# Performance work log

Measured on AMD Instinct MI355X. Metric: run time of the kernel, lower is better.

Reference implementation:

```python
import jax, jax.numpy as jnp
import numpy as np

NUM_EMBEDDINGS = 512
EMBEDDING_DIM = 64
COMMITMENT_COST = 0.25


def setup_inputs() -> dict:
    key = jax.random.key(0)
    k_in, k_cb = jax.random.split(key)
    inputs = jax.random.normal(k_in, (32, EMBEDDING_DIM, 64, 64), dtype=jnp.float32)
    # nn.Embedding weight initialized uniform(-1/K, 1/K)
    codebook = jax.random.uniform(
        k_cb, (NUM_EMBEDDINGS, EMBEDDING_DIM), dtype=jnp.float32,
        minval=-1.0 / NUM_EMBEDDINGS, maxval=1.0 / NUM_EMBEDDINGS)
    return {"inputs": inputs, "codebook": codebook}


def reference(inputs, codebook):
    N, D, H, W = inputs.shape
    # [N, H, W, D] -> [N*H*W, D]
    flat = jnp.transpose(inputs, (0, 2, 3, 1)).reshape(-1, D)
    # Squared euclidean distances (argmin identical to cdist's euclidean argmin)
    d2 = (jnp.sum(flat * flat, axis=1, keepdims=True)
          - 2.0 * flat @ codebook.T
          + jnp.sum(codebook * codebook, axis=1))  # [N*H*W, K]
    encoding_index = jnp.argmin(d2, axis=1)  # [N*H*W]
    quantized = codebook[encoding_index]      # gather [N*H*W, D]
    quantized = quantized.reshape(N, H, W, D).transpose(0, 3, 1, 2)  # [N, D, H, W]
    e_latent_loss = jnp.mean((jax.lax.stop_gradient(quantized) - inputs) ** 2)
    q_latent_loss = jnp.mean((quantized - jax.lax.stop_gradient(inputs)) ** 2)
    c_loss = q_latent_loss + COMMITMENT_COST * e_latent_loss
    # straight-through estimator
    quantized_st = inputs + jax.lax.stop_gradient(quantized - inputs)
    return (c_loss, quantized_st)
```

## Files before the change

### kernel.cpp

```cpp
#include <hip/hip_runtime.h>

#define DIM 64
#define HW 4096
#define NELEM 8388608.0f
#define NBLK 1024

typedef __attribute__((ext_vector_type(8))) short short8;
typedef __attribute__((ext_vector_type(4))) float f32x4;
typedef __attribute__((ext_vector_type(2))) float f32x2;

__device__ __forceinline__ unsigned short f2bf(float f) {
  unsigned int u = __builtin_bit_cast(unsigned int, f);
  u += 0x7fffu + ((u >> 16) & 1u);
  return (unsigned short)(u >> 16);
}

__device__ __forceinline__ float wave_sum(float v) {
  #pragma unroll
  for (int off = 32; off >= 1; off >>= 1) v += __shfl_xor(v, off);
  return v;
}


__global__ void vq_prep(const float* __restrict__ CB,
                        unsigned short* __restrict__ aFg,
                        float* __restrict__ cn) {
  const int t = threadIdx.x;
  const int s = blockIdx.x * 512 + t;
  const int chunk = s >> 7, ks = (s >> 6) & 1, ls = s & 63;
  const int code = chunk * 16 + (ls & 15);
  const int d0 = ks * 32 + (ls >> 4) * 8;
  const float* cp = CB + code * DIM + d0;
  float4 u0 = *(const float4*)cp;
  float4 u1 = *(const float4*)(cp + 4);
  short8 p;
  p[0]=(short)f2bf(-2.f*u0.x); p[1]=(short)f2bf(-2.f*u0.y);
  p[2]=(short)f2bf(-2.f*u0.z); p[3]=(short)f2bf(-2.f*u0.w);
  p[4]=(short)f2bf(-2.f*u1.x); p[5]=(short)f2bf(-2.f*u1.y);
  p[6]=(short)f2bf(-2.f*u1.z); p[7]=(short)f2bf(-2.f*u1.w);
  *(short8*)&aFg[s * 8] = p;
  if (blockIdx.x == 0) {
    const float* c2 = CB + t * DIM;
    float sn = 0.f;
    #pragma unroll
    for (int i = 0; i < 16; ++i) {
      float4 u = *(const float4*)(c2 + i * 4);
      sn += u.x*u.x + u.y*u.y + u.z*u.z + u.w*u.w;
    }
    cn[t] = sn;
  }
}

__global__ __launch_bounds__(256, 4)
void vq_main(const float* __restrict__ X, const float* __restrict__ CB,
             const unsigned short* __restrict__ aFg,
             const float* __restrict__ cng,
             float* __restrict__ out,
             float* __restrict__ pA, float* __restrict__ pB) {
  __shared__ __align__(16) unsigned short XF[16 * 64 * 8];
  __shared__ float mW[4][128];
  __shared__ float red[8];

  const int t   = threadIdx.x;
  const int bid = blockIdx.x;
  const int L   = ((bid & 7) << 7) | (bid >> 3);
  const int n   = L >> 5;
  const int hw0 = (L & 31) << 7;
  const int wv  = t >> 6, lane = t & 63;
  const int g   = lane >> 4, lcol = lane & 15;

  const float* Xg = X + n * (DIM * HW) + hw0;

  const int db8 = t >> 5;
  const int cp  = t & 31;
  const int kss = db8 >> 2, gs = db8 & 3;
  f32x2 v[2][8];
  #pragma unroll
  for (int h = 0; h < 2; ++h)
    #pragma unroll
    for (int j = 0; j < 8; ++j)
      v[h][j] = __builtin_nontemporal_load(
          (const f32x2*)(Xg + (db8 * 8 + j) * HW + h * 64 + cp * 2));
  float sx2 = 0.f;
  #pragma unroll
  for (int h = 0; h < 2; ++h)
    #pragma unroll
    for (int j = 0; j < 8; ++j)
      sx2 += v[h][j].x * v[h][j].x + v[h][j].y * v[h][j].y;
  #pragma unroll
  for (int h = 0; h < 2; ++h) {
    #pragma unroll
    for (int ci = 0; ci < 2; ++ci) {
      const int cl   = cp * 2 + ci;
      const int cb   = h * 4 + (cl >> 4);
      const int slot = (cb * 2 + kss) * 64 + gs * 16 + (cl & 15);
      const int swz  = slot ^ ((slot >> 3) & 7);
      short8 w;
      #pragma unroll
      for (int j = 0; j < 8; ++j)
        w[j] = (short)f2bf(ci ? v[h][j].y : v[h][j].x);
      *(short8*)&XF[swz * 8] = w;
    }
  }
  __syncthreads();

  const int swzl = lane ^ ((lane >> 3) & 7);
  short8 bfrag[2][4][2];
  #pragma unroll
  for (int h = 0; h < 2; ++h)
    #pragma unroll
    for (int cb2 = 0; cb2 < 4; ++cb2)
      #pragma unroll
      for (int ks = 0; ks < 2; ++ks)
        bfrag[h][cb2][ks] =
            *(const short8*)&XF[(((h * 4 + cb2) * 2 + ks) * 64 + swzl) * 8];

  float m1[8];
  #pragma unroll
  for (int cb = 0; cb < 8; ++cb) m1[cb] = 3.0e38f;

  const int chunk0 = wv * 8;
  #pragma unroll 2
  for (int i = 0; i < 8; ++i) {
    const int chunk = chunk0 + i;
    const short8 a0 = *(const short8*)&aFg[((chunk*2 + 0) * 64 + lane) * 8];
    const short8 a1 = *(const short8*)&aFg[((chunk*2 + 1) * 64 + lane) * 8];
    const int codebase = chunk * 16 + g * 4;
    const f32x4 cn = *(const f32x4*)&cng[codebase];
    #pragma unroll
    for (int h = 0; h < 2; ++h) {
      #pragma unroll
      for (int cb2 = 0; cb2 < 4; ++cb2) {
        f32x4 acc = cn;
        acc = __builtin_amdgcn_mfma_f32_16x16x32_bf16(a0, bfrag[h][cb2][0], acc, 0, 0, 0);
        acc = __builtin_amdgcn_mfma_f32_16x16x32_bf16(a1, bfrag[h][cb2][1], acc, 0, 0, 0);
        #pragma unroll
        for (int r = 0; r < 4; ++r) {
          unsigned int vb = __builtin_bit_cast(unsigned int, acc[r]);
          vb = (vb & 0xFFFFFE00u) | ((unsigned)(codebase + r) & 0x1FFu);
          m1[h * 4 + cb2] = fminf(m1[h * 4 + cb2], __builtin_bit_cast(float, vb));
        }
      }
    }
  }

  #pragma unroll
  for (int cb = 0; cb < 8; ++cb) {
    m1[cb] = fminf(m1[cb], __shfl_xor(m1[cb], 16));
    m1[cb] = fminf(m1[cb], __shfl_xor(m1[cb], 32));
    if (g == 0) mW[wv][cb * 16 + lcol] = m1[cb];
  }
  __syncthreads();

  float msum = 0.f;
  #pragma unroll
  for (int h = 0; h < 2; ++h) {
    const int c = h * 64 + lane;
    const float p = fminf(fminf(mW[0][c], mW[1][c]),
                          fminf(mW[2][c], mW[3][c]));
    const unsigned int b = __builtin_bit_cast(unsigned int, p);
    const int k = (int)(b & 511u);
    msum += __builtin_bit_cast(float, b & 0xFFFFFE00u);

    const float* cq = CB + k * DIM + wv * 16;
    float* op = out + 1 + n * (DIM * HW) + hw0 + c;
    #pragma unroll
    for (int i = 0; i < 4; ++i) {
      float4 u = *(const float4*)(cq + i * 4);
      __builtin_nontemporal_store(u.x, &op[(wv*16 + i*4 + 0) * HW]);
      __builtin_nontemporal_store(u.y, &op[(wv*16 + i*4 + 1) * HW]);
      __builtin_nontemporal_store(u.z, &op[(wv*16 + i*4 + 2) * HW]);
      __builtin_nontemporal_store(u.w, &op[(wv*16 + i*4 + 3) * HW]);
    }
  }

  float w1 = wave_sum(sx2);
  if (lane == 0) red[wv] = w1;
  if (wv == 0) {
    float w2 = wave_sum(msum);
    if (lane == 0) red[4] = w2;
  }
  __syncthreads();
  if (t == 0) {
    pA[bid] = red[0] + red[1] + red[2] + red[3];
    pB[bid] = red[4];
  }
}

__global__ void vq_fin(const float* __restrict__ pA,
                       const float* __restrict__ pB,
                       float* __restrict__ out) {
  const int t = threadIdx.x;
  f32x2 a = *(const f32x2*)&pA[t * 2];
  f32x2 c = *(const f32x2*)&pB[t * 2];
  float v = a.x + a.y + c.x + c.y;
  v = wave_sum(v);
  __shared__ float r[8];
  if ((t & 63) == 0) r[t >> 6] = v;
  __syncthreads();
  if (t == 0) {
    float s = 0.f;
    #pragma unroll
    for (int i = 0; i < 8; ++i) s += r[i];
    out[0] = 1.25f * s * (1.0f / NELEM);
  }
}

extern "C" void kernel_launch(void* const* d_in, const int* in_sizes, int n_in,
                              void* d_out, int out_size, void* d_ws, size_t ws_size,
                              hipStream_t stream) {
  const float* X  = (const float*)d_in[0];
  const float* CB = (const float*)d_in[1];
  float* out = (float*)d_out;
  char* ws = (char*)d_ws;
  unsigned short* aFg = (unsigned short*)ws;
  float* cn = (float*)(ws + 65536);
  float* pA = (float*)(ws + 67584);
  float* pB = (float*)(ws + 75776);
  (void)in_sizes; (void)n_in; (void)out_size; (void)ws_size;

  vq_prep<<<8, 512, 0, stream>>>(CB, aFg, cn);
  vq_main<<<NBLK, 256, 0, stream>>>(X, CB, aFg, cn, out, pA, pB);
  vq_fin<<<1, 512, 0, stream>>>(pA, pB, out);
}
```

Baseline: 34.25 us.

## Fuse codebook prep into main kernel, keep A fragments and norms in registers

Removes the separate vq_prep launch. Each block now loads its wave's codebook slice from global memory, converts it to bf16 MFMA A-fragments, and computes code norms with a shuffle reduction, all kept in registers. The loop is reordered so the h loop is outermost, which halves the live B fragments, and launch bounds drop to 3 blocks per SM to fit the extra registers. This saves one kernel launch and the workspace round trip, but every block redoes the codebook conversion and occupancy is lower.

```diff
diff --git a/kernel.cpp b/kernel.cpp
--- a/kernel.cpp
+++ b/kernel.cpp
@@ -22,39 +22,8 @@
 }
 
 
-__global__ void vq_prep(const float* __restrict__ CB,
-                        unsigned short* __restrict__ aFg,
-                        float* __restrict__ cn) {
-  const int t = threadIdx.x;
-  const int s = blockIdx.x * 512 + t;
-  const int chunk = s >> 7, ks = (s >> 6) & 1, ls = s & 63;
-  const int code = chunk * 16 + (ls & 15);
-  const int d0 = ks * 32 + (ls >> 4) * 8;
-  const float* cp = CB + code * DIM + d0;
-  float4 u0 = *(const float4*)cp;
-  float4 u1 = *(const float4*)(cp + 4);
-  short8 p;
-  p[0]=(short)f2bf(-2.f*u0.x); p[1]=(short)f2bf(-2.f*u0.y);
-  p[2]=(short)f2bf(-2.f*u0.z); p[3]=(short)f2bf(-2.f*u0.w);
-  p[4]=(short)f2bf(-2.f*u1.x); p[5]=(short)f2bf(-2.f*u1.y);
-  p[6]=(short)f2bf(-2.f*u1.z); p[7]=(short)f2bf(-2.f*u1.w);
-  *(short8*)&aFg[s * 8] = p;
-  if (blockIdx.x == 0) {
-    const float* c2 = CB + t * DIM;
-    float sn = 0.f;
-    #pragma unroll
-    for (int i = 0; i < 16; ++i) {
-      float4 u = *(const float4*)(c2 + i * 4);
-      sn += u.x*u.x + u.y*u.y + u.z*u.z + u.w*u.w;
-    }
-    cn[t] = sn;
-  }
-}
-
-__global__ __launch_bounds__(256, 4)
+__global__ __launch_bounds__(256, 3)
 void vq_main(const float* __restrict__ X, const float* __restrict__ CB,
-             const unsigned short* __restrict__ aFg,
-             const float* __restrict__ cng,
              float* __restrict__ out,
              float* __restrict__ pA, float* __restrict__ pB) {
   __shared__ __align__(16) unsigned short XF[16 * 64 * 8];
@@ -81,6 +50,32 @@
     for (int j = 0; j < 8; ++j)
       v[h][j] = __builtin_nontemporal_load(
           (const f32x2*)(Xg + (db8 * 8 + j) * HW + h * 64 + cp * 2));
+
+  short8 areg[8][2];
+  float cnv[8];
+  #pragma unroll
+  for (int i = 0; i < 8; ++i) {
+    const int code = (wv * 8 + i) * 16 + lcol;
+    float pc = 0.f;
+    #pragma unroll
+    for (int ks = 0; ks < 2; ++ks) {
+      const float* cpp = CB + code * DIM + ks * 32 + g * 8;
+      float4 u0 = *(const float4*)cpp;
+      float4 u1 = *(const float4*)(cpp + 4);
+      pc += u0.x*u0.x + u0.y*u0.y + u0.z*u0.z + u0.w*u0.w
+          + u1.x*u1.x + u1.y*u1.y + u1.z*u1.z + u1.w*u1.w;
+      short8 p;
+      p[0]=(short)f2bf(-2.f*u0.x); p[1]=(short)f2bf(-2.f*u0.y);
+      p[2]=(short)f2bf(-2.f*u0.z); p[3]=(short)f2bf(-2.f*u0.w);
+      p[4]=(short)f2bf(-2.f*u1.x); p[5]=(short)f2bf(-2.f*u1.y);
+      p[6]=(short)f2bf(-2.f*u1.z); p[7]=(short)f2bf(-2.f*u1.w);
+      areg[i][ks] = p;
+    }
+    pc += __shfl_xor(pc, 16);
+    pc += __shfl_xor(pc, 32);
+    cnv[i] = pc;
+  }
+
   float sx2 = 0.f;
   #pragma unroll
   for (int h = 0; h < 2; ++h)
@@ -104,36 +99,34 @@
   }
   __syncthreads();
 
+  float m1[8];
+  #pragma unroll
+  for (int cb = 0; cb < 8; ++cb) m1[cb] = 3.0e38f;
+
   const int swzl = lane ^ ((lane >> 3) & 7);
-  short8 bfrag[2][4][2];
-  #pragma unroll
-  for (int h = 0; h < 2; ++h)
+  #pragma unroll
+  for (int h = 0; h < 2; ++h) {
+    short8 bfrag[4][2];
     #pragma unroll
     for (int cb2 = 0; cb2 < 4; ++cb2)
       #pragma unroll
       for (int ks = 0; ks < 2; ++ks)
-        bfrag[h][cb2][ks] =
+        bfrag[cb2][ks] =
             *(const short8*)&XF[(((h * 4 + cb2) * 2 + ks) * 64 + swzl) * 8];
 
-  float m1[8];
-  #pragma unroll
-  for (int cb = 0; cb < 8; ++cb) m1[cb] = 3.0e38f;
-
-  const int chunk0 = wv * 8;
-  #pragma unroll 2
-  for (int i = 0; i < 8; ++i) {
-    const int chunk = chunk0 + i;
-    const short8 a0 = *(const short8*)&aFg[((chunk*2 + 0) * 64 + lane) * 8];
-    const short8 a1 = *(const short8*)&aFg[((chunk*2 + 1) * 64 + lane) * 8];
-    const int codebase = chunk * 16 + g * 4;
-    const f32x4 cn = *(const f32x4*)&cng[codebase];
-    #pragma unroll
-    for (int h = 0; h < 2; ++h) {
+    #pragma unroll
+    for (int i = 0; i < 8; ++i) {
+      const int codebase = (wv * 8 + i) * 16 + g * 4;
+      f32x4 cn;
+      cn[0] = __shfl(cnv[i], g * 4 + 0, 16);
+      cn[1] = __shfl(cnv[i], g * 4 + 1, 16);
+      cn[2] = __shfl(cnv[i], g * 4 + 2, 16);
+      cn[3] = __shfl(cnv[i], g * 4 + 3, 16);
       #pragma unroll
       for (int cb2 = 0; cb2 < 4; ++cb2) {
         f32x4 acc = cn;
-        acc = __builtin_amdgcn_mfma_f32_16x16x32_bf16(a0, bfrag[h][cb2][0], acc, 0, 0, 0);
-        acc = __builtin_amdgcn_mfma_f32_16x16x32_bf16(a1, bfrag[h][cb2][1], acc, 0, 0, 0);
+        acc = __builtin_amdgcn_mfma_f32_16x16x32_bf16(areg[i][0], bfrag[cb2][0], acc, 0, 0, 0);
+        acc = __builtin_amdgcn_mfma_f32_16x16x32_bf16(areg[i][1], bfrag[cb2][1], acc, 0, 0, 0);
         #pragma unroll
         for (int r = 0; r < 4; ++r) {
           unsigned int vb = __builtin_bit_cast(unsigned int, acc[r]);
@@ -213,13 +206,10 @@
   const float* CB = (const float*)d_in[1];
   float* out = (float*)d_out;
   char* ws = (char*)d_ws;
-  unsigned short* aFg = (unsigned short*)ws;
-  float* cn = (float*)(ws + 65536);
-  float* pA = (float*)(ws + 67584);
-  float* pB = (float*)(ws + 75776);
+  float* pA = (float*)ws;
+  float* pB = (float*)(ws + 4096);
   (void)in_sizes; (void)n_in; (void)out_size; (void)ws_size;
 
-  vq_prep<<<8, 512, 0, stream>>>(CB, aFg, cn);
-  vq_main<<<NBLK, 256, 0, stream>>>(X, CB, aFg, cn, out, pA, pB);
+  vq_main<<<NBLK, 256, 0, stream>>>(X, CB, out, pA, pB);
   vq_fin<<<1, 512, 0, stream>>>(pA, pB, out);
 }
```

Result: slower. 103.1 us (+200.9%).

## Enlarge per-block tile to 512 pixels with 8 waves splitting codebook

Applied to the files above, without the earlier changes.

Each block now handles 512 spatial positions with 512 threads instead of 128 positions with 256 threads, so only 256 blocks run. Each of the 8 waves owns 64 codes and keeps its A fragments and code norms in registers while it loops over 8 column groups. The aim is to reuse the codebook fragments across more pixels and cut how often aFg is refetched per block. Fewer blocks on a 256-CU part gives about one block per CU, which risks poorer latency hiding and higher LDS use per block.

```diff
diff --git a/kernel.cpp b/kernel.cpp
--- a/kernel.cpp
+++ b/kernel.cpp
@@ -3,7 +3,7 @@
 #define DIM 64
 #define HW 4096
 #define NELEM 8388608.0f
-#define NBLK 1024
+#define NBLK 256
 
 typedef __attribute__((ext_vector_type(8))) short short8;
 typedef __attribute__((ext_vector_type(4))) float f32x4;
@@ -51,126 +51,133 @@
   }
 }
 
-__global__ __launch_bounds__(256, 4)
+__global__ __launch_bounds__(512, 2)
 void vq_main(const float* __restrict__ X, const float* __restrict__ CB,
              const unsigned short* __restrict__ aFg,
              const float* __restrict__ cng,
              float* __restrict__ out,
              float* __restrict__ pA, float* __restrict__ pB) {
-  __shared__ __align__(16) unsigned short XF[16 * 64 * 8];
-  __shared__ float mW[4][128];
-  __shared__ float red[8];
+  __shared__ __align__(16) unsigned short XF[64 * 64 * 8];
+  __shared__ float mW[8][512];
+  __shared__ float red[16];
 
   const int t   = threadIdx.x;
   const int bid = blockIdx.x;
-  const int L   = ((bid & 7) << 7) | (bid >> 3);
-  const int n   = L >> 5;
-  const int hw0 = (L & 31) << 7;
+  const int L   = ((bid & 7) << 5) | (bid >> 3);
+  const int n   = L >> 3;
+  const int hw0 = (L & 7) << 9;
   const int wv  = t >> 6, lane = t & 63;
   const int g   = lane >> 4, lcol = lane & 15;
+  const int db8 = t >> 6;
+  const int cs  = lane;
+  const int kss = db8 >> 2, gs = db8 & 3;
 
   const float* Xg = X + n * (DIM * HW) + hw0;
 
-  const int db8 = t >> 5;
-  const int cp  = t & 31;
-  const int kss = db8 >> 2, gs = db8 & 3;
-  f32x2 v[2][8];
-  #pragma unroll
-  for (int h = 0; h < 2; ++h)
-    #pragma unroll
-    for (int j = 0; j < 8; ++j)
-      v[h][j] = __builtin_nontemporal_load(
-          (const f32x2*)(Xg + (db8 * 8 + j) * HW + h * 64 + cp * 2));
+  f32x2 v[8][4];
+  #pragma unroll
+  for (int j = 0; j < 8; ++j)
+    #pragma unroll
+    for (int q = 0; q < 4; ++q)
+      v[j][q] = __builtin_nontemporal_load(
+          (const f32x2*)(Xg + (db8 * 8 + j) * HW + q * 128 + cs * 2));
   float sx2 = 0.f;
   #pragma unroll
-  for (int h = 0; h < 2; ++h)
-    #pragma unroll
-    for (int j = 0; j < 8; ++j)
-      sx2 += v[h][j].x * v[h][j].x + v[h][j].y * v[h][j].y;
-  #pragma unroll
-  for (int h = 0; h < 2; ++h) {
+  for (int j = 0; j < 8; ++j)
+    #pragma unroll
+    for (int q = 0; q < 4; ++q)
+      sx2 += v[j][q].x * v[j][q].x + v[j][q].y * v[j][q].y;
+  #pragma unroll
+  for (int q = 0; q < 4; ++q) {
     #pragma unroll
     for (int ci = 0; ci < 2; ++ci) {
-      const int cl   = cp * 2 + ci;
-      const int cb   = h * 4 + (cl >> 4);
-      const int slot = (cb * 2 + kss) * 64 + gs * 16 + (cl & 15);
+      const int c    = q * 128 + cs * 2 + ci;
+      const int cb   = c >> 4;
+      const int slot = (cb * 2 + kss) * 64 + gs * 16 + (c & 15);
       const int swz  = slot ^ ((slot >> 3) & 7);
       short8 w;
       #pragma unroll
       for (int j = 0; j < 8; ++j)
-        w[j] = (short)f2bf(ci ? v[h][j].y : v[h][j].x);
+        w[j] = (short)f2bf(ci ? v[j][q].y : v[j][q].x);
       *(short8*)&XF[swz * 8] = w;
     }
   }
   __syncthreads();
 
   const int swzl = lane ^ ((lane >> 3) & 7);
-  short8 bfrag[2][4][2];
-  #pragma unroll
-  for (int h = 0; h < 2; ++h)
+  f32x4 cnq[4];
+  #pragma unroll
+  for (int i = 0; i < 4; ++i)
+    cnq[i] = *(const f32x4*)&cng[(wv * 4 + i) * 16 + g * 4];
+
+  #pragma unroll 1
+  for (int cg = 0; cg < 8; ++cg) {
+    short8 bfrag[4][2];
     #pragma unroll
     for (int cb2 = 0; cb2 < 4; ++cb2)
       #pragma unroll
       for (int ks = 0; ks < 2; ++ks)
-        bfrag[h][cb2][ks] =
-            *(const short8*)&XF[(((h * 4 + cb2) * 2 + ks) * 64 + swzl) * 8];
-
-  float m1[8];
-  #pragma unroll
-  for (int cb = 0; cb < 8; ++cb) m1[cb] = 3.0e38f;
-
-  const int chunk0 = wv * 8;
-  #pragma unroll 2
-  for (int i = 0; i < 8; ++i) {
-    const int chunk = chunk0 + i;
-    const short8 a0 = *(const short8*)&aFg[((chunk*2 + 0) * 64 + lane) * 8];
-    const short8 a1 = *(const short8*)&aFg[((chunk*2 + 1) * 64 + lane) * 8];
-    const int codebase = chunk * 16 + g * 4;
-    const f32x4 cn = *(const f32x4*)&cng[codebase];
-    #pragma unroll
-    for (int h = 0; h < 2; ++h) {
+        bfrag[cb2][ks] =
+            *(const short8*)&XF[(((cg * 4 + cb2) * 2 + ks) * 64 + swzl) * 8];
+
+    float m1[4];
+    #pragma unroll
+    for (int cb2 = 0; cb2 < 4; ++cb2) m1[cb2] = 3.0e38f;
+
+    #pragma unroll
+    for (int i = 0; i < 4; ++i) {
+      const int chunk = wv * 4 + i;
+      const short8 a0 = *(const short8*)&aFg[((chunk*2 + 0) * 64 + lane) * 8];
+      const short8 a1 = *(const short8*)&aFg[((chunk*2 + 1) * 64 + lane) * 8];
+      const int codebase = chunk * 16 + g * 4;
       #pragma unroll
       for (int cb2 = 0; cb2 < 4; ++cb2) {
-        f32x4 acc = cn;
-        acc = __builtin_amdgcn_mfma_f32_16x16x32_bf16(a0, bfrag[h][cb2][0], acc, 0, 0, 0);
-        acc = __builtin_amdgcn_mfma_f32_16x16x32_bf16(a1, bfrag[h][cb2][1], acc, 0, 0, 0);
+        f32x4 acc = cnq[i];
+        acc = __builtin_amdgcn_mfma_f32_16x16x32_bf16(a0, bfrag[cb2][0], acc, 0, 0, 0);
+        acc = __builtin_amdgcn_mfma_f32_16x16x32_bf16(a1, bfrag[cb2][1], acc, 0, 0, 0);
         #pragma unroll
         for (int r = 0; r < 4; ++r) {
           unsigned int vb = __builtin_bit_cast(unsigned int, acc[r]);
           vb = (vb & 0xFFFFFE00u) | ((unsigned)(codebase + r) & 0x1FFu);
-          m1[h * 4 + cb2] = fminf(m1[h * 4 + cb2], __builtin_bit_cast(float, vb));
+          m1[cb2] = fminf(m1[cb2], __builtin_bit_cast(float, vb));
         }
       }
     }
-  }
-
-  #pragma unroll
-  for (int cb = 0; cb < 8; ++cb) {
-    m1[cb] = fminf(m1[cb], __shfl_xor(m1[cb], 16));
-    m1[cb] = fminf(m1[cb], __shfl_xor(m1[cb], 32));
-    if (g == 0) mW[wv][cb * 16 + lcol] = m1[cb];
+    #pragma unroll
+    for (int cb2 = 0; cb2 < 4; ++cb2) {
+      m1[cb2] = fminf(m1[cb2], __shfl_xor(m1[cb2], 16));
+      m1[cb2] = fminf(m1[cb2], __shfl_xor(m1[cb2], 32));
+      if (g == 0) mW[wv][cg * 64 + cb2 * 16 + lcol] = m1[cb2];
+    }
   }
   __syncthreads();
 
   float msum = 0.f;
-  #pragma unroll
-  for (int h = 0; h < 2; ++h) {
-    const int c = h * 64 + lane;
-    const float p = fminf(fminf(mW[0][c], mW[1][c]),
-                          fminf(mW[2][c], mW[3][c]));
+  const float* cqp[8];
+  #pragma unroll
+  for (int hh = 0; hh < 8; ++hh) {
+    const int c = hh * 64 + lane;
+    float p = fminf(fminf(mW[0][c], mW[1][c]), fminf(mW[2][c], mW[3][c]));
+    p = fminf(p, fminf(fminf(mW[4][c], mW[5][c]), fminf(mW[6][c], mW[7][c])));
     const unsigned int b = __builtin_bit_cast(unsigned int, p);
     const int k = (int)(b & 511u);
     msum += __builtin_bit_cast(float, b & 0xFFFFFE00u);
-
-    const float* cq = CB + k * DIM + wv * 16;
-    float* op = out + 1 + n * (DIM * HW) + hw0 + c;
-    #pragma unroll
-    for (int i = 0; i < 4; ++i) {
-      float4 u = *(const float4*)(cq + i * 4);
-      __builtin_nontemporal_store(u.x, &op[(wv*16 + i*4 + 0) * HW]);
-      __builtin_nontemporal_store(u.y, &op[(wv*16 + i*4 + 1) * HW]);
-      __builtin_nontemporal_store(u.z, &op[(wv*16 + i*4 + 2) * HW]);
-      __builtin_nontemporal_store(u.w, &op[(wv*16 + i*4 + 3) * HW]);
+    cqp[hh] = CB + k * DIM + wv * 8;
+  }
+
+  float* opb = out + 1 + n * (DIM * HW) + hw0 + lane;
+  #pragma unroll
+  for (int i = 0; i < 2; ++i) {
+    f32x4 U[8];
+    #pragma unroll
+    for (int hh = 0; hh < 8; ++hh)
+      U[hh] = *(const f32x4*)(cqp[hh] + i * 4);
+    #pragma unroll
+    for (int rr = 0; rr < 4; ++rr) {
+      float* op = opb + (wv * 8 + i * 4 + rr) * HW;
+      #pragma unroll
+      for (int hh = 0; hh < 8; ++hh)
+        __builtin_nontemporal_store(U[hh][rr], &op[hh * 64]);
     }
   }
 
@@ -178,12 +185,15 @@
   if (lane == 0) red[wv] = w1;
   if (wv == 0) {
     float w2 = wave_sum(msum);
-    if (lane == 0) red[4] = w2;
+    if (lane == 0) red[8] = w2;
   }
   __syncthreads();
   if (t == 0) {
-    pA[bid] = red[0] + red[1] + red[2] + red[3];
-    pB[bid] = red[4];
+    float s = 0.f;
+    #pragma unroll
+    for (int i = 0; i < 8; ++i) s += red[i];
+    pA[bid] = s;
+    pB[bid] = red[8];
   }
 }
 
@@ -191,19 +201,13 @@
                        const float* __restrict__ pB,
                        float* __restrict__ out) {
   const int t = threadIdx.x;
-  f32x2 a = *(const f32x2*)&pA[t * 2];
-  f32x2 c = *(const f32x2*)&pB[t * 2];
-  float v = a.x + a.y + c.x + c.y;
+  float v = pA[t] + pB[t];
   v = wave_sum(v);
-  __shared__ float r[8];
+  __shared__ float r[4];
   if ((t & 63) == 0) r[t >> 6] = v;
   __syncthreads();
-  if (t == 0) {
-    float s = 0.f;
-    #pragma unroll
-    for (int i = 0; i < 8; ++i) s += r[i];
-    out[0] = 1.25f * s * (1.0f / NELEM);
-  }
+  if (t == 0)
+    out[0] = 1.25f * (r[0] + r[1] + r[2] + r[3]) * (1.0f / NELEM);
 }
 
 extern "C" void kernel_launch(void* const* d_in, const int* in_sizes, int n_in,
@@ -220,6 +224,6 @@
   (void)in_sizes; (void)n_in; (void)out_size; (void)ws_size;
 
   vq_prep<<<8, 512, 0, stream>>>(CB, aFg, cn);
-  vq_main<<<NBLK, 256, 0, stream>>>(X, CB, aFg, cn, out, pA, pB);
-  vq_fin<<<1, 512, 0, stream>>>(pA, pB, out);
-}
+  vq_main<<<NBLK, 512, 0, stream>>>(X, CB, aFg, cn, out, pA, pB);
+  vq_fin<<<1, 256, 0, stream>>>(pA, pB, out);
+}
```

After: 34.30 us. About the same (+0.1%).
